# Kernel optimization log

Hardware: AMD Instinct MI355X
Metric: run time of the kernel (lower is better)

## Reference

```python
import jax, jax.numpy as jnp
import numpy as np

N = 100000      # nodes
E = 1600000     # edges
F_IN = 128
HID = 64
N_CLS = 40


def setup_inputs() -> dict:
    key = jax.random.key(0)
    ks = jax.random.split(key, 8)
    x = jax.random.normal(ks[0], (N, F_IN), dtype=jnp.float32)
    edge_index = jax.random.randint(ks[1], (2, E), 0, N, dtype=jnp.int64)
    # SAGEConv params: lin_l (applied to mean-aggregated neighbors, with bias),
    # lin_r (applied to root/self features, no bias). Glorot-ish init scaling.
    W1_l = jax.random.normal(ks[2], (F_IN, HID), dtype=jnp.float32) / np.sqrt(F_IN)
    b1 = jnp.zeros((HID,), dtype=jnp.float32)
    W1_r = jax.random.normal(ks[3], (F_IN, HID), dtype=jnp.float32) / np.sqrt(F_IN)
    W2_l = jax.random.normal(ks[4], (HID, N_CLS), dtype=jnp.float32) / np.sqrt(HID)
    b2 = jnp.zeros((N_CLS,), dtype=jnp.float32)
    W2_r = jax.random.normal(ks[5], (HID, N_CLS), dtype=jnp.float32) / np.sqrt(HID)
    return {"x": x, "edge_index": edge_index,
            "W1_l": W1_l, "b1": b1, "W1_r": W1_r,
            "W2_l": W2_l, "b2": b2, "W2_r": W2_r}


def _sage_conv(x, src, dst, W_l, b_l, W_r):
    # mean aggregation of neighbor features: messages flow src -> dst
    msgs = x[src]                                              # [E, d]
    summed = jax.ops.segment_sum(msgs, dst, num_segments=N)    # [N, d]
    cnt = jax.ops.segment_sum(jnp.ones((src.shape[0],), x.dtype), dst,
                              num_segments=N)                  # [N]
    agg = summed / jnp.maximum(cnt, 1.0)[:, None]
    return agg @ W_l + b_l + x @ W_r


def reference(x, edge_index, W1_l, b1, W1_r, W2_l, b2, W2_r):
    src, dst = edge_index[0], edge_index[1]
    h = jax.nn.relu(_sage_conv(x, src, dst, W1_l, b1, W1_r))
    # dropout: identity in eval mode
    logits = _sage_conv(h, src, dst, W2_l, b2, W2_r)
    return jax.nn.log_softmax(logits, axis=1)
```

## Files before the change

kernel.cpp:

```cpp
#include <hip/hip_runtime.h>
#include <math.h>

#define N_NODES 100000
#define F_IN    128
#define HID     64
#define N_CLS   40
#define MT      (N_NODES / 16)

#define BSHIFT  9
#define BSZ     512
#define NB      ((N_NODES + BSZ - 1) / BSZ)
#define EPB     4096
#define CAP     9216

typedef __attribute__((ext_vector_type(8))) short bf8_t;
typedef __attribute__((ext_vector_type(4))) float f4_t;
typedef __attribute__((ext_vector_type(2))) float f2v_t;

typedef unsigned short ushort_t;
typedef unsigned int uint_t;
typedef unsigned char uchar_t;

__device__ __forceinline__ ushort_t f2b(float f) {
    union { float f; uint_t u; } c; c.f = f;
    uint_t u = c.u + 0x7FFFu + ((c.u >> 16) & 1u);
    return (ushort_t)(u >> 16);
}
__device__ __forceinline__ float b2f(ushort_t h) {
    union { uint_t u; float f; } c; c.u = ((uint_t)h) << 16;
    return c.f;
}

#if defined(__has_builtin)
#if __has_builtin(__builtin_amdgcn_cvt_pk_f32_fp8) && __has_builtin(__builtin_amdgcn_cvt_pk_fp8_f32)
#define HAVE_FP8_HW 1
#endif
#endif

__device__ __forceinline__ uchar_t fp8_enc(float v) {
#ifdef HAVE_FP8_HW
    return (uchar_t)(__builtin_amdgcn_cvt_pk_fp8_f32(v, v, 0, false) & 0xff);
#else
    union { float f; uint_t u; } c; c.f = v;
    uint_t s = c.u >> 31;
    float av = fabsf(v);
    if (av > 448.f) av = 448.f;
    int e;
    float m = frexpf(av, &e);
    int ee = e + 6;
    uchar_t r;
    if (av == 0.f) r = 0;
    else if (ee <= 0) {
        int q = (int)(av * 512.f + 0.5f);
        if (q > 7) q = 7;
        r = (uchar_t)q;
    } else {
        int q = (int)(m * 16.f + 0.5f);
        if (q == 16) { q = 8; ee += 1; }
        if (ee > 15) { ee = 15; q = 15; }
        r = (uchar_t)((ee << 3) | (q & 7));
    }
    return r | (uchar_t)(s << 7);
#endif
}

__device__ __forceinline__ f2v_t fp8x2_dec_lo(uint_t w) {
#ifdef HAVE_FP8_HW
    return __builtin_amdgcn_cvt_pk_f32_fp8(w, false);
#else
    f2v_t r;
    for (int k = 0; k < 2; ++k) {
        uchar_t b = (w >> (8 * k)) & 0xff;
        uint_t s = (b >> 7) & 1, e = (b >> 3) & 15, m = b & 7;
        float f;
        if (e) { union { uint_t u; float ff; } c;
                 c.u = (s << 31) | ((e + 120) << 23) | (m << 20); f = c.ff; }
        else   { f = (float)m * 0.001953125f; if (s) f = -f; }
        r[k] = f;
    }
    return r;
#endif
}
__device__ __forceinline__ f2v_t fp8x2_dec_hi(uint_t w) {
#ifdef HAVE_FP8_HW
    return __builtin_amdgcn_cvt_pk_f32_fp8(w, true);
#else
    return fp8x2_dec_lo(w >> 16);
#endif
}

__global__ void init_cvt_kernel(const float* __restrict__ W1l,
                                const float* __restrict__ W1r,
                                const float* __restrict__ W2l,
                                const float* __restrict__ W2r,
                                ushort_t* __restrict__ W1t,
                                ushort_t* __restrict__ W2t,
                                int* __restrict__ gcur) {
    int t = blockIdx.x * blockDim.x + threadIdx.x;
    if (t < NB) gcur[t] = 0;
    if (t < 128 * F_IN) {
        int n = t / F_IN, k = t - n * F_IN;
        float v = (n < HID) ? W1l[k * HID + n] : W1r[k * HID + (n - HID)];
        W1t[t] = f2b(v);
    } else if (t < 128 * F_IN + 80 * HID) {
        int u = t - 128 * F_IN;
        int n = u / HID, k = u - n * HID;
        float v = (n < N_CLS) ? W2l[k * N_CLS + n] : W2r[k * N_CLS + (n - N_CLS)];
        W2t[u] = f2b(v);
    }
}

__global__ void scatter_direct_kernel(const int* __restrict__ ei, int E,
                                      int* __restrict__ gcur,
                                      uint_t* __restrict__ arena) {
    __shared__ int cnt[NB];
    __shared__ int rbase[NB];
    __shared__ int cur[NB];
    int t = threadIdx.x, blk = blockIdx.x;
    for (int i = t; i < NB; i += 256) { cnt[i] = 0; cur[i] = 0; }
    __syncthreads();
    int e0 = blk * EPB;
#pragma unroll
    for (int i = 0; i < EPB / 256; ++i) {
        int e = e0 + i * 256 + t;
        if (e < E) atomicAdd(&cnt[ei[E + e] >> BSHIFT], 1);
    }
    __syncthreads();
    for (int i = t; i < NB; i += 256) {
        int c = cnt[i];
        rbase[i] = c ? atomicAdd(&gcur[i], c) : 0;
    }
    __syncthreads();
#pragma unroll
    for (int i = 0; i < EPB / 256; ++i) {
        int e = e0 + i * 256 + t;
        if (e < E) {
            int src = ei[e];
            int dst = ei[E + e];
            int bin = dst >> BSHIFT;
            int r = atomicAdd(&cur[bin], 1);
            arena[(size_t)bin * CAP + rbase[bin] + r] =
                ((uint_t)src << BSHIFT) | (uint_t)(dst & (BSZ - 1));
        }
    }
}

__global__ void bucket_sort_kernel(const uint_t* __restrict__ arena,
                                   const int* __restrict__ gcur,
                                   int* __restrict__ rowptr,
                                   int* __restrict__ csr) {
    __shared__ int hist[BSZ];
    __shared__ int lofs[BSZ];
    int bin = blockIdx.x, t = threadIdx.x;
    int pv = (t < NB) ? gcur[t] : 0;
    lofs[t] = pv;
    __syncthreads();
    for (int off = 1; off < BSZ; off <<= 1) {
        int u = (t >= off) ? lofs[t - off] : 0;
        __syncthreads();
        lofs[t] += u;
        __syncthreads();
    }
    int base = (bin > 0) ? lofs[bin - 1] : 0;
    int cnt = gcur[bin];
    __syncthreads();
    hist[t] = 0;
    __syncthreads();
    const uint_t* ap = arena + (size_t)bin * CAP;
    for (int i = t; i < cnt; i += BSZ)
        atomicAdd(&hist[ap[i] & (BSZ - 1)], 1);
    __syncthreads();
    int v = hist[t];
    lofs[t] = v;
    __syncthreads();
    for (int off = 1; off < BSZ; off <<= 1) {
        int u = (t >= off) ? lofs[t - off] : 0;
        __syncthreads();
        lofs[t] += u;
        __syncthreads();
    }
    int excl = lofs[t] - v;
    int d_global = (bin << BSHIFT) + t;
    if (d_global < N_NODES) rowptr[d_global] = base + excl;
    if (bin == NB - 1 && t == 0) rowptr[N_NODES] = base + cnt;
    __syncthreads();
    lofs[t] = excl;
    hist[t] = 0;
    __syncthreads();
    for (int i = t; i < cnt; i += BSZ) {
        uint_t p = ap[i];
        int lb = p & (BSZ - 1);
        int r = atomicAdd(&hist[lb], 1);
        csr[base + lofs[lb] + r] = (int)(p >> BSHIFT);
    }
}

__global__ void gemm1_mfma_kernel(const float* __restrict__ x,
                                  const ushort_t* __restrict__ W1t,
                                  uchar_t* __restrict__ y1f8,
                                  ushort_t* __restrict__ z1b) {
    __shared__ uchar_t sy[128][80];
    __shared__ ushort_t sz[128][72];
    int tid = threadIdx.x;
    int wave = tid >> 6, lane = tid & 63;
    int tile0 = blockIdx.x * 8 + wave * 2;
    int m0b = blockIdx.x * 128;
    int r = lane & 15, q = lane >> 4;
    bool v0 = (tile0 < MT), v1 = (tile0 + 1 < MT);

    bf8_t a0[4], a1[4];
#pragma unroll
    for (int kt = 0; kt < 4; ++kt) { a0[kt] = (bf8_t)(short)0; a1[kt] = (bf8_t)(short)0; }
    if (v0) {
        const float* xr = x + (size_t)(tile0 * 16 + r) * F_IN + q * 8;
#pragma unroll
        for (int kt = 0; kt < 4; ++kt) {
            float4 u = *(const float4*)(xr + kt * 32);
            float4 v = *(const float4*)(xr + kt * 32 + 4);
            bf8_t tt;
            tt[0] = (short)f2b(u.x); tt[1] = (short)f2b(u.y);
            tt[2] = (short)f2b(u.z); tt[3] = (short)f2b(u.w);
            tt[4] = (short)f2b(v.x); tt[5] = (short)f2b(v.y);
            tt[6] = (short)f2b(v.z); tt[7] = (short)f2b(v.w);
            a0[kt] = tt;
        }
    }
    if (v1) {
        const float* xr = x + (size_t)((tile0 + 1) * 16 + r) * F_IN + q * 8;
#pragma unroll
        for (int kt = 0; kt < 4; ++kt) {
            float4 u = *(const float4*)(xr + kt * 32);
            float4 v = *(const float4*)(xr + kt * 32 + 4);
            bf8_t tt;
            tt[0] = (short)f2b(u.x); tt[1] = (short)f2b(u.y);
            tt[2] = (short)f2b(u.z); tt[3] = (short)f2b(u.w);
            tt[4] = (short)f2b(v.x); tt[5] = (short)f2b(v.y);
            tt[6] = (short)f2b(v.z); tt[7] = (short)f2b(v.w);
            a1[kt] = tt;
        }
    }
    int lr0 = wave * 32 + q * 4;
#pragma unroll
    for (int tn = 0; tn < 8; ++tn) {
        const ushort_t* wr = W1t + (size_t)(tn * 16 + r) * F_IN + q * 8;
        bf8_t b[4];
#pragma unroll
        for (int kt = 0; kt < 4; ++kt)
            b[kt] = *(const bf8_t*)(wr + kt * 32);
        f4_t acc0 = {0.f, 0.f, 0.f, 0.f};
        f4_t acc1 = {0.f, 0.f, 0.f, 0.f};
#pragma unroll
        for (int kt = 0; kt < 4; ++kt) {
            acc0 = __builtin_amdgcn_mfma_f32_16x16x32_bf16(a0[kt], b[kt], acc0, 0, 0, 0);
            acc1 = __builtin_amdgcn_mfma_f32_16x16x32_bf16(a1[kt], b[kt], acc1, 0, 0, 0);
        }
        int col = tn * 16 + r;
        if (col < 64) {
            if (v0) {
#pragma unroll
                for (int rr = 0; rr < 4; ++rr) sy[lr0 + rr][col] = fp8_enc(acc0[rr]);
            }
            if (v1) {
#pragma unroll
                for (int rr = 0; rr < 4; ++rr) sy[lr0 + 16 + rr][col] = fp8_enc(acc1[rr]);
            }
        } else {
            if (v0) {
#pragma unroll
                for (int rr = 0; rr < 4; ++rr) sz[lr0 + rr][col - 64] = f2b(acc0[rr]);
            }
            if (v1) {
#pragma unroll
                for (int rr = 0; rr < 4; ++rr) sz[lr0 + 16 + rr][col - 64] = f2b(acc1[rr]);
            }
        }
    }
    __syncthreads();
    int vrows = N_NODES - m0b; if (vrows > 128) vrows = 128;
    for (int idx = tid; idx < vrows * 4; idx += 256) {
        int row = idx >> 2, c = (idx & 3) << 4;
        *(uint4*)(y1f8 + (size_t)(m0b + row) * 64 + c) = *(const uint4*)&sy[row][c];
    }
    for (int idx = tid; idx < vrows * 8; idx += 256) {
        int row = idx >> 3, c = (idx & 7) << 3;
        *(uint4*)(z1b + (size_t)(m0b + row) * HID + c) = *(const uint4*)&sz[row][c];
    }
}

__device__ __forceinline__ void acc16(float* acc, uint4 v) {
    f2v_t p;
    p = fp8x2_dec_lo(v.x); acc[0]  += p[0]; acc[1]  += p[1];
    p = fp8x2_dec_hi(v.x); acc[2]  += p[0]; acc[3]  += p[1];
    p = fp8x2_dec_lo(v.y); acc[4]  += p[0]; acc[5]  += p[1];
    p = fp8x2_dec_hi(v.y); acc[6]  += p[0]; acc[7]  += p[1];
    p = fp8x2_dec_lo(v.z); acc[8]  += p[0]; acc[9]  += p[1];
    p = fp8x2_dec_hi(v.z); acc[10] += p[0]; acc[11] += p[1];
    p = fp8x2_dec_lo(v.w); acc[12] += p[0]; acc[13] += p[1];
    p = fp8x2_dec_hi(v.w); acc[14] += p[0]; acc[15] += p[1];
}

__global__ void agg1_kernel(const int* __restrict__ rowptr,
                            const int* __restrict__ csr,
                            const uchar_t* __restrict__ y1f8,
                            const ushort_t* __restrict__ z1b,
                            const float* __restrict__ b1,
                            ushort_t* __restrict__ hb,
                            uchar_t* __restrict__ hf8) {
    int gid = blockIdx.x * blockDim.x + threadIdx.x;
    int wave = gid >> 6, lane = gid & 63;
    int g = lane >> 2, l = lane & 3;
    int n = wave * 16 + g;
    if (n >= N_NODES) return;
    int beg = rowptr[n], end = rowptr[n + 1];
    float acc[16];
#pragma unroll
    for (int j = 0; j < 16; ++j) acc[j] = 0.f;
    const uchar_t* yb = y1f8 + l * 16;
    int i = beg;
    for (; i + 3 < end; i += 4) {
        int s0 = csr[i], s1 = csr[i + 1], s2 = csr[i + 2], s3 = csr[i + 3];
        uint4 w0 = *(const uint4*)(yb + (size_t)s0 * 64);
        uint4 w1 = *(const uint4*)(yb + (size_t)s1 * 64);
        uint4 w2 = *(const uint4*)(yb + (size_t)s2 * 64);
        uint4 w3 = *(const uint4*)(yb + (size_t)s3 * 64);
        acc16(acc, w0); acc16(acc, w1); acc16(acc, w2); acc16(acc, w3);
    }
    for (; i < end; ++i) {
        uint4 w = *(const uint4*)(yb + (size_t)csr[i] * 64);
        acc16(acc, w);
    }
    float inv = 1.0f / fmaxf((float)(end - beg), 1.0f);
    int c = l * 16;
    ushort_t zz[16];
    *(uint4*)&zz[0] = *(const uint4*)(z1b + (size_t)n * HID + c);
    *(uint4*)&zz[8] = *(const uint4*)(z1b + (size_t)n * HID + c + 8);
    float bv[16];
    *(float4*)&bv[0]  = *(const float4*)(b1 + c);
    *(float4*)&bv[4]  = *(const float4*)(b1 + c + 4);
    *(float4*)&bv[8]  = *(const float4*)(b1 + c + 8);
    *(float4*)&bv[12] = *(const float4*)(b1 + c + 12);
    ushort_t o[16];
    uchar_t of[16];
#pragma unroll
    for (int j = 0; j < 16; ++j) {
        float r = fmaxf(fmaf(acc[j], inv, bv[j] + b2f(zz[j])), 0.f);
        o[j] = f2b(r);
        of[j] = fp8_enc(r);
    }
    *(uint4*)(hb + (size_t)n * HID + c)     = *(const uint4*)&o[0];
    *(uint4*)(hb + (size_t)n * HID + c + 8) = *(const uint4*)&o[8];
    *(uint4*)(hf8 + (size_t)n * 64 + c)     = *(const uint4*)&of[0];
}

__global__ void layer2_fused_kernel(const int* __restrict__ rowptr,
                                    const int* __restrict__ csr,
                                    const uchar_t* __restrict__ hf8,
                                    const ushort_t* __restrict__ hb,
                                    const ushort_t* __restrict__ W2t,
                                    const float* __restrict__ b2,
                                    float* __restrict__ out) {
    __shared__ ushort_t sA[64][72];
    __shared__ float sO[64][44];
    int tid = threadIdx.x;
    int wave = tid >> 6, lane = tid & 63;
    int m0b = blockIdx.x * 64;
    int tileN = m0b + wave * 16;
    bool valid = (tileN < N_NODES);

    if (valid) {
        int g = lane >> 2, l = lane & 3;
        int n = tileN + g;
        int beg = rowptr[n], end = rowptr[n + 1];
        float acc[16];
#pragma unroll
        for (int j = 0; j < 16; ++j) acc[j] = 0.f;
        const uchar_t* yb = hf8 + l * 16;
        int i = beg;
        for (; i + 3 < end; i += 4) {
            int s0 = csr[i], s1 = csr[i + 1], s2 = csr[i + 2], s3 = csr[i + 3];
            uint4 w0 = *(const uint4*)(yb + (size_t)s0 * 64);
            uint4 w1 = *(const uint4*)(yb + (size_t)s1 * 64);
            uint4 w2 = *(const uint4*)(yb + (size_t)s2 * 64);
            uint4 w3 = *(const uint4*)(yb + (size_t)s3 * 64);
            acc16(acc, w0); acc16(acc, w1); acc16(acc, w2); acc16(acc, w3);
        }
        for (; i < end; ++i) {
            uint4 w = *(const uint4*)(yb + (size_t)csr[i] * 64);
            acc16(acc, w);
        }
        float inv = 1.0f / fmaxf((float)(end - beg), 1.0f);
        ushort_t o[16];
#pragma unroll
        for (int j = 0; j < 16; ++j)
            o[j] = f2b(acc[j] * inv);
        int lrow = wave * 16 + g;
        *(uint4*)&sA[lrow][l * 16]     = *(const uint4*)&o[0];
        *(uint4*)&sA[lrow][l * 16 + 8] = *(const uint4*)&o[8];
    }
    __syncthreads();
    if (valid) {
        int r = lane & 15, q = lane >> 4;
        const ushort_t* ar = &sA[wave * 16 + r][q * 8];
        const ushort_t* hr = hb + (size_t)(tileN + r) * HID + q * 8;
        bf8_t a0[2], a1[2];
#pragma unroll
        for (int kt = 0; kt < 2; ++kt) {
            a0[kt] = *(const bf8_t*)(ar + kt * 32);
            a1[kt] = *(const bf8_t*)(hr + kt * 32);
        }
        float v[3][4];
#pragma unroll
        for (int tn = 0; tn < 3; ++tn) {
            int col = tn * 16 + r;
            int cl = (col < N_CLS) ? col : 0;
            const ushort_t* wl  = W2t + (size_t)cl * HID + q * 8;
            const ushort_t* wr2 = W2t + (size_t)(N_CLS + cl) * HID + q * 8;
            f4_t acc4 = {0.f, 0.f, 0.f, 0.f};
#pragma unroll
            for (int kt = 0; kt < 2; ++kt) {
                bf8_t bl = *(const bf8_t*)(wl + kt * 32);
                acc4 = __builtin_amdgcn_mfma_f32_16x16x32_bf16(a0[kt], bl, acc4, 0, 0, 0);
            }
#pragma unroll
            for (int kt = 0; kt < 2; ++kt) {
                bf8_t br = *(const bf8_t*)(wr2 + kt * 32);
                acc4 = __builtin_amdgcn_mfma_f32_16x16x32_bf16(a1[kt], br, acc4, 0, 0, 0);
            }
            float bias = (col < N_CLS) ? b2[cl] : 0.f;
#pragma unroll
            for (int rr = 0; rr < 4; ++rr)
                v[tn][rr] = (col < N_CLS) ? (acc4[rr] + bias) : -INFINITY;
        }
        int lrow = wave * 16 + q * 4;
#pragma unroll
        for (int rr = 0; rr < 4; ++rr) {
            float m = fmaxf(fmaxf(v[0][rr], v[1][rr]), v[2][rr]);
#pragma unroll
            for (int off = 1; off < 16; off <<= 1)
                m = fmaxf(m, __shfl_xor(m, off, 64));
            float s = 0.f;
#pragma unroll
            for (int tn = 0; tn < 3; ++tn)
                if (v[tn][rr] > -INFINITY) s += expf(v[tn][rr] - m);
#pragma unroll
            for (int off = 1; off < 16; off <<= 1)
                s += __shfl_xor(s, off, 64);
            float ls = m + logf(s);
#pragma unroll
            for (int tn = 0; tn < 3; ++tn) {
                int col = tn * 16 + r;
                if (col < N_CLS)
                    sO[lrow + rr][col] = v[tn][rr] - ls;
            }
        }
    }
    __syncthreads();
    int vrows = N_NODES - m0b; if (vrows > 64) vrows = 64;
    for (int idx = tid; idx < vrows * 10; idx += 256) {
        int row = idx / 10, c = (idx - row * 10) * 4;
        *(float4*)(out + (size_t)(m0b + row) * N_CLS + c) = *(const float4*)&sO[row][c];
    }
}

extern "C" void kernel_launch(void* const* d_in, const int* in_sizes, int n_in,
                              void* d_out, int out_size, void* d_ws, size_t ws_size,
                              hipStream_t stream) {
    const float* x   = (const float*)d_in[0];
    const int*   ei  = (const int*)d_in[1];
    const float* W1l = (const float*)d_in[2];
    const float* b1  = (const float*)d_in[3];
    const float* W1r = (const float*)d_in[4];
    const float* W2l = (const float*)d_in[5];
    const float* b2  = (const float*)d_in[6];
    const float* W2r = (const float*)d_in[7];
    float* out = (float*)d_out;
    const int E = in_sizes[1] / 2;
    const int nblk = (E + EPB - 1) / EPB;

    char* p = (char*)d_ws;
    auto take = [&](size_t bytes) {
        char* q = p;
        p += (bytes + 15) & ~(size_t)15;
        return (void*)q;
    };
    int* rowptr     = (int*)take(sizeof(int) * (N_NODES + 4));
    int* gcur       = (int*)take(sizeof(int) * NB);
    uint_t* arena   = (uint_t*)take(sizeof(uint_t) * (size_t)NB * CAP);
    int* csr        = (int*)take(sizeof(int) * (size_t)E);
    ushort_t* W1t   = (ushort_t*)take(sizeof(ushort_t) * 128 * F_IN);
    ushort_t* W2t   = (ushort_t*)take(sizeof(ushort_t) * 80 * HID);
    uchar_t* y1f8   = (uchar_t*)take(sizeof(uchar_t) * (size_t)N_NODES * 64);
    ushort_t* z1b   = (ushort_t*)take(sizeof(ushort_t) * (size_t)N_NODES * HID);
    ushort_t* hb    = (ushort_t*)take(sizeof(ushort_t) * (size_t)N_NODES * HID);
    uchar_t* hf8    = (uchar_t*)take(sizeof(uchar_t) * (size_t)N_NODES * 64);

    const int B = 256;

    init_cvt_kernel<<<(128 * F_IN + 80 * HID + B - 1) / B, B, 0, stream>>>(
        W1l, W1r, W2l, W2r, W1t, W2t, gcur);
    scatter_direct_kernel<<<nblk, 256, 0, stream>>>(ei, E, gcur, arena);
    bucket_sort_kernel<<<NB, BSZ, 0, stream>>>(arena, gcur, rowptr, csr);

    int gemm1_blocks = (MT + 7) / 8;
    int l2_blocks = (N_NODES + 63) / 64;
    int t_agg = (N_NODES / 16) * 64;

    gemm1_mfma_kernel<<<gemm1_blocks, B, 0, stream>>>(x, W1t, y1f8, z1b);
    agg1_kernel<<<(t_agg + B - 1) / B, B, 0, stream>>>(rowptr, csr, y1f8, z1b, b1, hb, hf8);
    layer2_fused_kernel<<<l2_blocks, B, 0, stream>>>(rowptr, csr, hf8, hb, W2t, b2, out);
}
```

Measured before the change: 244.0 us.

## Split layer-2 fused aggregate+GEMM kernel into separate aggregation and GEMM kernels

Replaces the single layer-2 kernel that aggregated neighbor features into shared memory and then ran the MFMA GEMM plus log-softmax with two kernels. The first writes the mean-aggregated bf16 features to a new global buffer; the second reads that buffer and runs the GEMM, bias and log-softmax. The aim is to free the gather phase from the shared-memory footprint and the __syncthreads barrier, which should improve occupancy and latency hiding. The cost is an extra global round-trip of N×64 bf16 values and one more kernel launch.

```diff
diff --git a/kernel.cpp b/kernel.cpp
--- a/kernel.cpp
+++ b/kernel.cpp
@@ -352,60 +352,62 @@
     *(uint4*)(hf8 + (size_t)n * 64 + c)     = *(const uint4*)&of[0];
 }
 
-__global__ void layer2_fused_kernel(const int* __restrict__ rowptr,
-                                    const int* __restrict__ csr,
-                                    const uchar_t* __restrict__ hf8,
-                                    const ushort_t* __restrict__ hb,
-                                    const ushort_t* __restrict__ W2t,
-                                    const float* __restrict__ b2,
-                                    float* __restrict__ out) {
-    __shared__ ushort_t sA[64][72];
-    __shared__ float sO[64][44];
+__global__ void agg2m_kernel(const int* __restrict__ rowptr,
+                             const int* __restrict__ csr,
+                             const uchar_t* __restrict__ hf8,
+                             ushort_t* __restrict__ mb) {
+    int gid = blockIdx.x * blockDim.x + threadIdx.x;
+    int wave = gid >> 6, lane = gid & 63;
+    int g = lane >> 2, l = lane & 3;
+    int n = wave * 16 + g;
+    if (n >= N_NODES) return;
+    int beg = rowptr[n], end = rowptr[n + 1];
+    float acc[16];
+#pragma unroll
+    for (int j = 0; j < 16; ++j) acc[j] = 0.f;
+    const uchar_t* yb = hf8 + l * 16;
+    int i = beg;
+    for (; i + 3 < end; i += 4) {
+        int s0 = csr[i], s1 = csr[i + 1], s2 = csr[i + 2], s3 = csr[i + 3];
+        uint4 w0 = *(const uint4*)(yb + (size_t)s0 * 64);
+        uint4 w1 = *(const uint4*)(yb + (size_t)s1 * 64);
+        uint4 w2 = *(const uint4*)(yb + (size_t)s2 * 64);
+        uint4 w3 = *(const uint4*)(yb + (size_t)s3 * 64);
+        acc16(acc, w0); acc16(acc, w1); acc16(acc, w2); acc16(acc, w3);
+    }
+    for (; i < end; ++i) {
+        uint4 w = *(const uint4*)(yb + (size_t)csr[i] * 64);
+        acc16(acc, w);
+    }
+    float inv = 1.0f / fmaxf((float)(end - beg), 1.0f);
+    int c = l * 16;
+    ushort_t o[16];
+#pragma unroll
+    for (int j = 0; j < 16; ++j)
+        o[j] = f2b(acc[j] * inv);
+    *(uint4*)(mb + (size_t)n * HID + c)     = *(const uint4*)&o[0];
+    *(uint4*)(mb + (size_t)n * HID + c + 8) = *(const uint4*)&o[8];
+}
+
+__global__ void gemm2_fused_kernel(const ushort_t* __restrict__ mb,
+                                   const ushort_t* __restrict__ hb,
+                                   const ushort_t* __restrict__ W2t,
+                                   const float* __restrict__ b2,
+                                   float* __restrict__ out) {
+    __shared__ float sOut[64][44];
     int tid = threadIdx.x;
     int wave = tid >> 6, lane = tid & 63;
+    int tile = blockIdx.x * 4 + wave;
     int m0b = blockIdx.x * 64;
-    int tileN = m0b + wave * 16;
-    bool valid = (tileN < N_NODES);
-
-    if (valid) {
-        int g = lane >> 2, l = lane & 3;
-        int n = tileN + g;
-        int beg = rowptr[n], end = rowptr[n + 1];
-        float acc[16];
-#pragma unroll
-        for (int j = 0; j < 16; ++j) acc[j] = 0.f;
-        const uchar_t* yb = hf8 + l * 16;
-        int i = beg;
-        for (; i + 3 < end; i += 4) {
-            int s0 = csr[i], s1 = csr[i + 1], s2 = csr[i + 2], s3 = csr[i + 3];
-            uint4 w0 = *(const uint4*)(yb + (size_t)s0 * 64);
-            uint4 w1 = *(const uint4*)(yb + (size_t)s1 * 64);
-            uint4 w2 = *(const uint4*)(yb + (size_t)s2 * 64);
-            uint4 w3 = *(const uint4*)(yb + (size_t)s3 * 64);
-            acc16(acc, w0); acc16(acc, w1); acc16(acc, w2); acc16(acc, w3);
-        }
-        for (; i < end; ++i) {
-            uint4 w = *(const uint4*)(yb + (size_t)csr[i] * 64);
-            acc16(acc, w);
-        }
-        float inv = 1.0f / fmaxf((float)(end - beg), 1.0f);
-        ushort_t o[16];
-#pragma unroll
-        for (int j = 0; j < 16; ++j)
-            o[j] = f2b(acc[j] * inv);
-        int lrow = wave * 16 + g;
-        *(uint4*)&sA[lrow][l * 16]     = *(const uint4*)&o[0];
-        *(uint4*)&sA[lrow][l * 16 + 8] = *(const uint4*)&o[8];
-    }
-    __syncthreads();
-    if (valid) {
+    if (tile < MT) {
+        int m0 = tile * 16;
         int r = lane & 15, q = lane >> 4;
-        const ushort_t* ar = &sA[wave * 16 + r][q * 8];
-        const ushort_t* hr = hb + (size_t)(tileN + r) * HID + q * 8;
+        const ushort_t* mr = mb + (size_t)(m0 + r) * HID + q * 8;
+        const ushort_t* hr = hb + (size_t)(m0 + r) * HID + q * 8;
         bf8_t a0[2], a1[2];
 #pragma unroll
         for (int kt = 0; kt < 2; ++kt) {
-            a0[kt] = *(const bf8_t*)(ar + kt * 32);
+            a0[kt] = *(const bf8_t*)(mr + kt * 32);
             a1[kt] = *(const bf8_t*)(hr + kt * 32);
         }
         float v[3][4];
@@ -413,23 +415,23 @@
         for (int tn = 0; tn < 3; ++tn) {
             int col = tn * 16 + r;
             int cl = (col < N_CLS) ? col : 0;
-            const ushort_t* wl  = W2t + (size_t)cl * HID + q * 8;
-            const ushort_t* wr2 = W2t + (size_t)(N_CLS + cl) * HID + q * 8;
-            f4_t acc4 = {0.f, 0.f, 0.f, 0.f};
+            const ushort_t* wl = W2t + (size_t)cl * HID + q * 8;
+            const ushort_t* wrp = W2t + (size_t)(N_CLS + cl) * HID + q * 8;
+            f4_t acc = {0.f, 0.f, 0.f, 0.f};
 #pragma unroll
             for (int kt = 0; kt < 2; ++kt) {
                 bf8_t bl = *(const bf8_t*)(wl + kt * 32);
-                acc4 = __builtin_amdgcn_mfma_f32_16x16x32_bf16(a0[kt], bl, acc4, 0, 0, 0);
+                acc = __builtin_amdgcn_mfma_f32_16x16x32_bf16(a0[kt], bl, acc, 0, 0, 0);
             }
 #pragma unroll
             for (int kt = 0; kt < 2; ++kt) {
-                bf8_t br = *(const bf8_t*)(wr2 + kt * 32);
-                acc4 = __builtin_amdgcn_mfma_f32_16x16x32_bf16(a1[kt], br, acc4, 0, 0, 0);
+                bf8_t br = *(const bf8_t*)(wrp + kt * 32);
+                acc = __builtin_amdgcn_mfma_f32_16x16x32_bf16(a1[kt], br, acc, 0, 0, 0);
             }
             float bias = (col < N_CLS) ? b2[cl] : 0.f;
 #pragma unroll
             for (int rr = 0; rr < 4; ++rr)
-                v[tn][rr] = (col < N_CLS) ? (acc4[rr] + bias) : -INFINITY;
+                v[tn][rr] = (col < N_CLS) ? (acc[rr] + bias) : -INFINITY;
         }
         int lrow = wave * 16 + q * 4;
 #pragma unroll
@@ -450,7 +452,7 @@
             for (int tn = 0; tn < 3; ++tn) {
                 int col = tn * 16 + r;
                 if (col < N_CLS)
-                    sO[lrow + rr][col] = v[tn][rr] - ls;
+                    sOut[lrow + rr][col] = v[tn][rr] - ls;
             }
         }
     }
@@ -458,7 +460,7 @@
     int vrows = N_NODES - m0b; if (vrows > 64) vrows = 64;
     for (int idx = tid; idx < vrows * 10; idx += 256) {
         int row = idx / 10, c = (idx - row * 10) * 4;
-        *(float4*)(out + (size_t)(m0b + row) * N_CLS + c) = *(const float4*)&sO[row][c];
+        *(float4*)(out + (size_t)(m0b + row) * N_CLS + c) = *(const float4*)&sOut[row][c];
     }
 }
 
@@ -493,6 +495,7 @@
     ushort_t* z1b   = (ushort_t*)take(sizeof(ushort_t) * (size_t)N_NODES * HID);
     ushort_t* hb    = (ushort_t*)take(sizeof(ushort_t) * (size_t)N_NODES * HID);
     uchar_t* hf8    = (uchar_t*)take(sizeof(uchar_t) * (size_t)N_NODES * 64);
+    ushort_t* mb    = (ushort_t*)take(sizeof(ushort_t) * (size_t)N_NODES * HID);
 
     const int B = 256;
 
@@ -502,10 +505,11 @@
     bucket_sort_kernel<<<NB, BSZ, 0, stream>>>(arena, gcur, rowptr, csr);
 
     int gemm1_blocks = (MT + 7) / 8;
-    int l2_blocks = (N_NODES + 63) / 64;
+    int gemm2_blocks = (MT + 3) / 4;
     int t_agg = (N_NODES / 16) * 64;
 
     gemm1_mfma_kernel<<<gemm1_blocks, B, 0, stream>>>(x, W1t, y1f8, z1b);
     agg1_kernel<<<(t_agg + B - 1) / B, B, 0, stream>>>(rowptr, csr, y1f8, z1b, b1, hb, hf8);
-    layer2_fused_kernel<<<l2_blocks, B, 0, stream>>>(rowptr, csr, hf8, hb, W2t, b2, out);
-}
+    agg2m_kernel<<<(t_agg + B - 1) / B, B, 0, stream>>>(rowptr, csr, hf8, mb);
+    gemm2_fused_kernel<<<gemm2_blocks, B, 0, stream>>>(mb, hb, W2t, b2, out);
+}
```

New measurement: 250.9 us. 2.8% more time.
